# Kernel optimization log

Measured on AMD Instinct MI355X. Metric: run time of the kernel, lower is better.

The kernel has to match this reference:

```python
import jax, jax.numpy as jnp
import numpy as np

B, T, D = 2, 2048, 1024
NH, NKV, HD = 16, 4, 64
BASE, TSL, QGI = 10000.0, 1024, 1.5
EPS = 1.1920929e-07  # torch.finfo(float32).eps used by F.rms_norm default


def _rope_cos_sin(seq_len, rd):
    # Rotary.forward with self.rd == head_dim (Attn sets rd=0 -> full rotation)
    if seq_len > TSL:  # NTK-style base rescale branch
        nb = BASE * (seq_len / TSL) ** (rd / (rd - 2))
    else:
        nb = BASE
    inv = 1.0 / nb ** (jnp.arange(0, rd, 2, dtype=jnp.float32) / rd)
    fr = jnp.arange(seq_len, dtype=jnp.float32)[:, None] * inv[None, :]
    return jnp.cos(fr)[None, :, None, :], jnp.sin(fr)[None, :, None, :]


def _apply_rope(x, cos, sin):
    h = x.shape[-1] // 2
    x1, x2 = x[..., :h], x[..., h:]
    return jnp.concatenate([x1 * cos + x2 * sin, -x1 * sin + x2 * cos], axis=-1)


def _rms_norm(x):
    return x * jax.lax.rsqrt(jnp.mean(x * x, axis=-1, keepdims=True) + EPS)


def setup_inputs() -> dict:
    key = jax.random.key(0)
    ks = jax.random.split(key, 8)
    s = jnp.float32(0.02)
    return {
        "x": jax.random.normal(ks[0], (B, T, D), jnp.float32),
        "qw": jax.random.normal(ks[1], (NH * HD, D), jnp.float32) * s,
        "kw": jax.random.normal(ks[2], (NKV * HD, D), jnp.float32) * s,
        "vw": jax.random.normal(ks[3], (NKV * HD, D), jnp.float32) * s,
        "ow": jax.random.normal(ks[4], (D, D), jnp.float32) * s,
        "ve": jax.random.normal(ks[5], (B, T, NKV * HD), jnp.float32) * s,
        "v0": jax.random.normal(ks[6], (B, T, NKV, HD), jnp.float32) * s,
        "q_gain": jnp.full((NH,), QGI, jnp.float32),
        "vr_lambda": jnp.array([0.5, 0.5], jnp.float32),
        "gate_w": jnp.zeros((NH, D), jnp.float32),      # nn.init.zeros_
        "gate_b": jnp.full((NH,), 4.0, jnp.float32),    # nn.init.constant_(4.0)
    }


def reference(x, qw, kw, vw, ow, ve, v0, q_gain, vr_lambda, gate_w, gate_b):
    # projections
    q = (x @ qw.T).reshape(B, T, NH, HD)
    k = (x @ kw.T).reshape(B, T, NKV, HD)
    v = (x @ vw.T + ve).reshape(B, T, NKV, HD)
    raw_v = v  # returned when vr=True
    v = vr_lambda[0] * v0 + vr_lambda[1] * v  # value residual
    # qk rms-norm + rope (full head dim since self.rd == 0) + per-head q gain
    q = _rms_norm(q)
    k = _rms_norm(k)
    cos, sin = _rope_cos_sin(T, HD)
    q = _apply_rope(q, cos, sin)
    k = _apply_rope(k, cos, sin)
    q = q * q_gain[None, None, :, None]
    # causal GQA attention (nh query heads share nkv kv heads)
    G = NH // NKV
    qg = q.reshape(B, T, NKV, G, HD)
    scale = 1.0 / np.sqrt(HD).astype(np.float32)
    scores = jnp.einsum('bqhgd,bkhd->bhgqk', qg, k) * scale  # [B,NKV,G,T,T]
    causal = jnp.tril(jnp.ones((T, T), bool))
    scores = jnp.where(causal[None, None, None], scores, jnp.finfo(scores.dtype).min)
    p = jax.nn.softmax(scores, axis=-1)
    y = jnp.einsum('bhgqk,bkhd->bqhgd', p, v).reshape(B, T, NH, HD)
    # gated attention output
    gate = jax.nn.sigmoid(x @ gate_w.T + gate_b)  # [B,T,NH]
    y = y * gate[..., None]
    out = y.reshape(B, T, D) @ ow.T
    return out, raw_v
```

## Files before the change

### kernel.cpp

```cpp
#include <hip/hip_runtime.h>
#include <math.h>

#define BB 2
#define TT 2048
#define DD 1024
#define NH 16
#define NKV 4
#define HD 64
#define EPSF 1.1920929e-07f
#define LOG2_NB 14.319970444065578
#define SCALE_LOG2E 0.18033688011112042f
#define FIXMAX 17.5f

typedef __attribute__((ext_vector_type(8))) short bf16x8;
typedef __attribute__((ext_vector_type(4))) float f32x4;

__device__ inline short f2bf(float f) {
    unsigned u = __builtin_bit_cast(unsigned, f);
    unsigned r = (u + 0x7fffu + ((u >> 16) & 1u)) >> 16;
    return (short)r;
}
__device__ inline float bf2f(short s) {
    unsigned u = ((unsigned)(unsigned short)s) << 16;
    return __builtin_bit_cast(float, u);
}
__device__ inline unsigned cvt_pk_bf16(float a, float b) {
    unsigned r;
    asm("v_cvt_pk_bf16_f32 %0, %1, %2" : "=v"(r) : "v"(a), "v"(b));
    return r;
}

__global__ __launch_bounds__(256) void conv_all(
    const float* __restrict__ x, const float* __restrict__ qw,
    const float* __restrict__ kw, const float* __restrict__ vw,
    const float* __restrict__ ow, const float* __restrict__ gw,
    short* __restrict__ x16, short* __restrict__ wb16, short* __restrict__ ow16)
{
    int i = blockIdx.x * 256 + threadIdx.x;
    if (i >= 1708032) {
        ((short4*)(wb16 + 1552*1024))[i - 1708032] = (short4){0,0,0,0};
        return;
    }
    const float* src; short* dst; int j;
    if (i < 1048576)      { src = x;  dst = x16;            j = i; }
    else if (i < 1310720) { src = qw; dst = wb16;           j = i - 1048576; }
    else if (i < 1376256) { src = kw; dst = wb16 + 1048576; j = i - 1310720; }
    else if (i < 1441792) { src = vw; dst = wb16 + 1310720; j = i - 1376256; }
    else if (i < 1703936) { src = ow; dst = ow16;           j = i - 1441792; }
    else                  { src = gw; dst = wb16 + 1572864; j = i - 1703936; }
    float4 v = ((const float4*)src)[j];
    short4 o;
    o.x = f2bf(v.x); o.y = f2bf(v.y); o.z = f2bf(v.z); o.w = f2bf(v.w);
    ((short4*)dst)[j] = o;
}

#define GSTAGE(buf, k0, Abase, Bbase)                                                   \
{                                                                                       \
    _Pragma("unroll")                                                                   \
    for (int i_ = 0; i_ < 2; i_++) {                                                    \
        int off = w*2048 + i_*1024;                      \
        int g = (off >> 4) + lane;                                   \
        int row = g >> 2, c = g & 3;                                                    \
        int cg = c ^ (row & 3);                                        \
        const short* ga = (Abase) + (size_t)(m0 + row)*1024 + (k0) + cg*8;              \
        __builtin_amdgcn_global_load_lds(                                               \
            (const __attribute__((address_space(1))) void*)ga,                          \
            (__attribute__((address_space(3))) void*)((char*)&As[buf][0] + off), 16, 0, 0); \
        const short* gb = (Bbase) + (size_t)(n0 + row)*1024 + (k0) + cg*8;              \
        __builtin_amdgcn_global_load_lds(                                               \
            (const __attribute__((address_space(1))) void*)gb,                          \
            (__attribute__((address_space(3))) void*)((char*)&Bs[buf][0] + off), 16, 0, 0); \
    }                                                                                   \
}

#define GEMM_MAIN_LOOP(kbeg, kend, Abase, Bbase)                                        \
    GSTAGE(0, (kbeg), (Abase), (Bbase));                                                \
    __syncthreads();                                                                    \
    for (int k0 = (kbeg); k0 < (kend); k0 += 32) {                                      \
        int cur = ((k0 - (kbeg)) >> 5) & 1;                                             \
        bf16x8 af[4], bfr[4];                                                           \
        _Pragma("unroll")                                                               \
        for (int tm = 0; tm < 4; tm++) {                                                \
            int row = wy*64 + tm*16 + lc;                                               \
            af[tm] = *(const bf16x8*)(&As[cur][0] + row*32 + ((quad*8) ^ ((row&3)*8))); \
        }                                                                               \
        _Pragma("unroll")                                                               \
        for (int tn = 0; tn < 4; tn++) {                                                \
            int row = wx*64 + tn*16 + lc;                                               \
            bfr[tn] = *(const bf16x8*)(&Bs[cur][0] + row*32 + ((quad*8) ^ ((row&3)*8))); \
        }                                                                               \
        if (k0 + 32 < (kend)) GSTAGE(cur ^ 1, k0 + 32, (Abase), (Bbase));               \
        _Pragma("unroll")                                                               \
        for (int tm = 0; tm < 4; tm++)                                                  \
            _Pragma("unroll")                                                           \
            for (int tn = 0; tn < 4; tn++)                                              \
                acc[tm][tn] = __builtin_amdgcn_mfma_f32_16x16x32_bf16(af[tm], bfr[tn], acc[tm][tn], 0, 0, 0); \
        __syncthreads();                                                                \
    }

__global__ __launch_bounds__(256, 3) void gemm_qkv_fused(
    const short* __restrict__ A, const short* __restrict__ Bmat,
    const float* __restrict__ ve, const float* __restrict__ v0,
    const float* __restrict__ q_gain, const float* __restrict__ vr_lambda,
    const float* __restrict__ gb_, float* __restrict__ gate,
    short* __restrict__ qbh, short* __restrict__ kbh, short* __restrict__ vtb,
    float* __restrict__ rawv)
{
    __shared__ short As[2][128*32];
    __shared__ short Bs[2][128*32];
    int tid = threadIdx.x;
    int w = tid >> 6, lane = tid & 63;
    int quad = lane >> 4, lc = lane & 15;
    int wy = w >> 1, wx = w & 1;
    int m0 = blockIdx.y * 128, n0 = blockIdx.x * 128;

    f32x4 acc[4][4];
    #pragma unroll
    for (int i = 0; i < 4; i++)
        #pragma unroll
        for (int j = 0; j < 4; j++) acc[i][j] = (f32x4){0.f,0.f,0.f,0.f};

    GEMM_MAIN_LOOP(0, 1024, A, Bmat);

    int hc = n0 + wx*64;
    if (hc < 1280) {
        bool isq = (hc < 1024);
        int h = isq ? (hc >> 6) : ((hc - 1024) >> 6);
        float gsc = isq ? (q_gain[h] * SCALE_LOG2E) : 1.0f;
        short* dst = isq ? qbh : kbh;
        int nhh = isq ? 16 : 4;
        float inv0 = (float)exp2((double)lc * (-LOG2_NB / 32.0));
        float inv1 = (float)exp2((double)(lc + 16) * (-LOG2_NB / 32.0));
        #pragma unroll
        for (int tm = 0; tm < 4; tm++) {
            #pragma unroll
            for (int r = 0; r < 4; r++) {
                int m = m0 + wy*64 + tm*16 + quad*4 + r;
                int b = m >> 11, t = m & (TT - 1);
                float a0 = acc[tm][0][r], a1 = acc[tm][1][r];
                float a2 = acc[tm][2][r], a3 = acc[tm][3][r];
                float ss = a0*a0 + a1*a1 + a2*a2 + a3*a3;
                ss += __shfl_xor(ss, 1);
                ss += __shfl_xor(ss, 2);
                ss += __shfl_xor(ss, 4);
                ss += __shfl_xor(ss, 8);
                float rn = rsqrtf(ss * (1.0f/64.0f) + EPSF);
                a0 *= rn; a1 *= rn; a2 *= rn; a3 *= rn;
                float sn0, cs0, sn1, cs1;
                sincosf((float)t * inv0, &sn0, &cs0);
                sincosf((float)t * inv1, &sn1, &cs1);
                float o0 = a0*cs0 + a2*sn0;
                float o1 = a1*cs1 + a3*sn1;
                float o2 = a2*cs0 - a0*sn0;
                float o3 = a3*cs1 - a1*sn1;
                size_t base = (((size_t)(b*nhh + h))*2048 + t)*64 + lc;
                dst[base +  0] = f2bf(o0 * gsc);
                dst[base + 16] = f2bf(o1 * gsc);
                dst[base + 32] = f2bf(o2 * gsc);
                dst[base + 48] = f2bf(o3 * gsc);
            }
        }
    } else if (hc < 1536) {
        int kvh = (hc - 1280) >> 6;
        float l0 = vr_lambda[0], l1 = vr_lambda[1];
        short* lbase = (w < 2) ? &As[w][0] : &Bs[w - 2][0];
        #pragma unroll
        for (int tm = 0; tm < 4; tm++) {
            #pragma unroll
            for (int r = 0; r < 4; r++) {
                int m = m0 + wy*64 + tm*16 + quad*4 + r;
                int tl = tm*16 + quad*4 + r;
                size_t off = (size_t)m*256 + kvh*64 + lc;
                #pragma unroll
                for (int tn = 0; tn < 4; tn++) {
                    int d = tn*16 + lc;
                    float val = acc[tm][tn][r] + ve[off + tn*16];
                    rawv[off + tn*16] = val;
                    lbase[d*64 + (tl ^ ((d & 7) * 8))] = f2bf(l0 * v0[off + tn*16] + l1 * val);
                }
            }
        }
        int b = m0 >> 11;
        int t0g = (m0 & 2047) + wy*64;
        short* vdst = vtb + (size_t)(b*4 + kvh)*64*2048;
        #pragma unroll
        for (int j = 0; j < 16; j++) {
            int d = quad + j*4;
            int tc = lc*4;
            short4 vv = *(const short4*)&lbase[d*64 + (tc ^ ((d & 7) * 8))];
            *(short4*)&vdst[(size_t)d*2048 + t0g + tc] = vv;
        }
    } else if (hc == 1536) {
        #pragma unroll
        for (int tm = 0; tm < 4; tm++)
            #pragma unroll
            for (int r = 0; r < 4; r++) {
                int m = m0 + wy*64 + tm*16 + quad*4 + r;
                float lg = acc[tm][0][r] + gb_[lc];
                gate[(size_t)m*16 + lc] = 1.0f / (1.0f + __expf(-lg));
            }
    }
}

__global__ __launch_bounds__(256, 4) void gemm_mfma(
    const short* __restrict__ A, const short* __restrict__ Bmat,
    float* __restrict__ C, int ldc, int klen)
{
    __shared__ short As[2][128*32];
    __shared__ short Bs[2][128*32];
    int tid = threadIdx.x;
    int w = tid >> 6, lane = tid & 63;
    int quad = lane >> 4, lc = lane & 15;
    int wy = w >> 1, wx = w & 1;
    int m0 = blockIdx.y * 128, n0 = blockIdx.x * 128;

    f32x4 acc[4][4];
    #pragma unroll
    for (int i = 0; i < 4; i++)
        #pragma unroll
        for (int j = 0; j < 4; j++) acc[i][j] = (f32x4){0.f,0.f,0.f,0.f};

    GEMM_MAIN_LOOP(0, klen, A, Bmat);

    #pragma unroll
    for (int tm = 0; tm < 4; tm++)
        #pragma unroll
        for (int r = 0; r < 4; r++) {
            int m = m0 + wy*64 + tm*16 + quad*4 + r;
            #pragma unroll
            for (int tn = 0; tn < 4; tn++) {
                int n = n0 + wx*64 + tn*16 + lc;
                C[(size_t)m*ldc + n] = acc[tm][tn][r];
            }
        }
}

__global__ __launch_bounds__(256, 4) void flash_mfma(
    const short* __restrict__ qbh, const short* __restrict__ kbh,
    const short* __restrict__ vtb, const float* __restrict__ gate,
    short* __restrict__ y16)
{
    __shared__ short Ks[2][64*64];
    __shared__ short Vt[2][64*64];
    __shared__ short Ps[4][16*64];

    int bh = blockIdx.x;
    int b = bh >> 4, h = bh & 15, kvh = h >> 2;
    int qt = 31 - blockIdx.y;
    int tid = threadIdx.x;
    int w = tid >> 6, lane = tid & 63;
    int quad = lane >> 4, lc = lane & 15;

    const short* qbase = qbh + (((size_t)bh)*2048 + qt*64 + w*16 + lc)*64;
    bf16x8 qf0 = *(const bf16x8*)(qbase + quad*8);
    bf16x8 qf1 = *(const bf16x8*)(qbase + 32 + quad*8);

    f32x4 o[4];
    #pragma unroll
    for (int i = 0; i < 4; i++) o[i] = (f32x4){0.f,0.f,0.f,0.f};
    f32x4 l4 = (f32x4){0.f,0.f,0.f,0.f};
    const bf16x8 ones = {(short)0x3F80,(short)0x3F80,(short)0x3F80,(short)0x3F80,
                         (short)0x3F80,(short)0x3F80,(short)0x3F80,(short)0x3F80};

    const size_t kbase = ((size_t)(b*4 + kvh))*2048*64;
    const size_t vbase = ((size_t)(b*4 + kvh))*64*2048;

    #define STAGE(buf, kt)                                                              \
    {                                                                                   \
        _Pragma("unroll")                                                               \
        for (int i = 0; i < 2; i++) {                                                   \
            int off = w*2048 + i*1024;                                                  \
            int g = (off >> 4) + lane;                                                  \
            int row = g >> 3, c = g & 7;                                                \
            int cg = c ^ (row & 7);                                                     \
            const short* gk = kbh + kbase + (size_t)((kt)*64 + row)*64 + cg*8;          \
            __builtin_amdgcn_global_load_lds(                                           \
                (const __attribute__((address_space(1))) void*)gk,                      \
                (__attribute__((address_space(3))) void*)((char*)Ks[buf] + off), 16, 0, 0); \
            const short* gv = vtb + vbase + (size_t)row*2048 + (kt)*64 + cg*8;          \
            __builtin_amdgcn_global_load_lds(                                           \
                (const __attribute__((address_space(1))) void*)gv,                      \
                (__attribute__((address_space(3))) void*)((char*)Vt[buf] + off), 16, 0, 0); \
        }                                                                               \
    }

    STAGE(0, 0);
    __syncthreads();

    short* ps = Ps[w];

    for (int kt = 0; kt <= qt; kt++) {
        int cur = kt & 1;
        bool diag = (kt == qt);

        bf16x8 kf0[4], kf1[4], vf0[4], vf1[4];
        #pragma unroll
        for (int kn = 0; kn < 4; kn++) {
            int row = kn*16 + lc;
            int sw = (row & 7) * 8;
            const short* kr = Ks[cur] + row*64;
            kf0[kn] = *(const bf16x8*)(kr + ((quad*8) ^ sw));
            kf1[kn] = *(const bf16x8*)(kr + ((quad*8 + 32) ^ sw));
            const short* vr = Vt[cur] + row*64;
            vf0[kn] = *(const bf16x8*)(vr + ((quad*8) ^ sw));
            vf1[kn] = *(const bf16x8*)(vr + ((quad*8 + 32) ^ sw));
        }
        if (kt < qt) STAGE(cur ^ 1, kt + 1);

        f32x4 s4[4];
        #pragma unroll
        for (int kn = 0; kn < 4; kn++) {
            f32x4 acc = (f32x4){0.f,0.f,0.f,0.f};
            acc = __builtin_amdgcn_mfma_f32_16x16x32_bf16(kf0[kn], qf0, acc, 0, 0, 0);
            acc = __builtin_amdgcn_mfma_f32_16x16x32_bf16(kf1[kn], qf1, acc, 0, 0, 0);
            s4[kn] = acc;
        }

        #pragma unroll
        for (int kn = 0; kn < 4; kn++) {
            float p0 = __builtin_amdgcn_exp2f(s4[kn][0] - FIXMAX);
            float p1 = __builtin_amdgcn_exp2f(s4[kn][1] - FIXMAX);
            float p2 = __builtin_amdgcn_exp2f(s4[kn][2] - FIXMAX);
            float p3 = __builtin_amdgcn_exp2f(s4[kn][3] - FIXMAX);
            if (diag) {
                int keyb = kn*16 + quad*4, qv = w*16 + lc;
                if (keyb + 0 > qv) p0 = 0.f;
                if (keyb + 1 > qv) p1 = 0.f;
                if (keyb + 2 > qv) p2 = 0.f;
                if (keyb + 3 > qv) p3 = 0.f;
            }
            int c = kn*4 + quad;
            int cs = c ^ ((lc & 7) << 1);
            int2 pk;
            pk.x = (int)cvt_pk_bf16(p0, p1);
            pk.y = (int)cvt_pk_bf16(p2, p3);
            *(int2*)(ps + lc*64 + cs*4) = pk;
        }
        __asm__ volatile("s_waitcnt lgkmcnt(0)" ::: "memory");
        int u0 = (0*4 + quad) ^ (lc & 7);
        int u1 = (1*4 + quad) ^ (lc & 7);
        bf16x8 pf0 = *(const bf16x8*)(ps + lc*64 + u0*8);
        bf16x8 pf1 = *(const bf16x8*)(ps + lc*64 + u1*8);

        #pragma unroll
        for (int dn = 0; dn < 4; dn++) {
            o[dn] = __builtin_amdgcn_mfma_f32_16x16x32_bf16(pf0, vf0[dn], o[dn], 0, 0, 0);
            o[dn] = __builtin_amdgcn_mfma_f32_16x16x32_bf16(pf1, vf1[dn], o[dn], 0, 0, 0);
        }
        l4 = __builtin_amdgcn_mfma_f32_16x16x32_bf16(pf0, ones, l4, 0, 0, 0);
        l4 = __builtin_amdgcn_mfma_f32_16x16x32_bf16(pf1, ones, l4, 0, 0, 0);
        __syncthreads();
    }

    #pragma unroll
    for (int r = 0; r < 4; r++) {
        int row = b*2048 + qt*64 + w*16 + quad*4 + r;
        float g = gate[(size_t)row*16 + h] / l4[r];
        #pragma unroll
        for (int dn = 0; dn < 4; dn++)
            y16[(size_t)row*1024 + h*64 + dn*16 + lc] = f2bf(o[dn][r] * g);
    }
}

extern "C" void kernel_launch(void* const* d_in, const int* in_sizes, int n_in,
                              void* d_out, int out_size, void* d_ws, size_t ws_size,
                              hipStream_t stream) {
    (void)in_sizes; (void)n_in; (void)out_size; (void)ws_size;
    const float* x  = (const float*)d_in[0];
    const float* qw = (const float*)d_in[1];
    const float* kw = (const float*)d_in[2];
    const float* vw = (const float*)d_in[3];
    const float* ow = (const float*)d_in[4];
    const float* ve = (const float*)d_in[5];
    const float* v0 = (const float*)d_in[6];
    const float* qg = (const float*)d_in[7];
    const float* vl = (const float*)d_in[8];
    const float* gw = (const float*)d_in[9];
    const float* gb = (const float*)d_in[10];

    float* out  = (float*)d_out;
    float* rawv = out + (size_t)BB*TT*DD;

    float* p    = (float*)d_ws;
    short* x16  = (short*)p;        p += 2097152;
    short* wb16 = (short*)p;        p += 851968;
    short* ow16 = (short*)p;        p += 524288;
    short* qbh  = (short*)p;        p += 2097152;
    short* kbh  = (short*)p;        p += 524288;
    short* vtb  = (short*)p;        p += 524288;
    float* gt   = p;                p += 65536;
    short* y16  = (short*)p;

    conv_all<<<6784, 256, 0, stream>>>(x, qw, kw, vw, ow, gw, x16, wb16, ow16);
    gemm_qkv_fused<<<dim3(13, 32), 256, 0, stream>>>(x16, wb16, ve, v0, qg, vl,
                                                     gb, gt, qbh, kbh, vtb, rawv);
    flash_mfma<<<dim3(32, 32), 256, 0, stream>>>(qbh, kbh, vtb, gt, y16);
    gemm_mfma<<<dim3(8, 32), 256, 0, stream>>>(y16, ow16, out, 1024, 1024);
}
```

Before: 186.1 us.

## Fuse fp32-to-bf16 conversion into QKV GEMM staging and drop conv kernel

Result: no change. 184.5 us (-0.9%).

```diff
diff --git a/kernel.cpp b/kernel.cpp
--- a/kernel.cpp
+++ b/kernel.cpp
@@ -20,38 +20,10 @@
     unsigned r = (u + 0x7fffu + ((u >> 16) & 1u)) >> 16;
     return (short)r;
 }
-__device__ inline float bf2f(short s) {
-    unsigned u = ((unsigned)(unsigned short)s) << 16;
-    return __builtin_bit_cast(float, u);
-}
 __device__ inline unsigned cvt_pk_bf16(float a, float b) {
     unsigned r;
     asm("v_cvt_pk_bf16_f32 %0, %1, %2" : "=v"(r) : "v"(a), "v"(b));
     return r;
-}
-
-__global__ __launch_bounds__(256) void conv_all(
-    const float* __restrict__ x, const float* __restrict__ qw,
-    const float* __restrict__ kw, const float* __restrict__ vw,
-    const float* __restrict__ ow, const float* __restrict__ gw,
-    short* __restrict__ x16, short* __restrict__ wb16, short* __restrict__ ow16)
-{
-    int i = blockIdx.x * 256 + threadIdx.x;
-    if (i >= 1708032) {
-        ((short4*)(wb16 + 1552*1024))[i - 1708032] = (short4){0,0,0,0};
-        return;
-    }
-    const float* src; short* dst; int j;
-    if (i < 1048576)      { src = x;  dst = x16;            j = i; }
-    else if (i < 1310720) { src = qw; dst = wb16;           j = i - 1048576; }
-    else if (i < 1376256) { src = kw; dst = wb16 + 1048576; j = i - 1310720; }
-    else if (i < 1441792) { src = vw; dst = wb16 + 1310720; j = i - 1376256; }
-    else if (i < 1703936) { src = ow; dst = ow16;           j = i - 1441792; }
-    else                  { src = gw; dst = wb16 + 1572864; j = i - 1703936; }
-    float4 v = ((const float4*)src)[j];
-    short4 o;
-    o.x = f2bf(v.x); o.y = f2bf(v.y); o.z = f2bf(v.z); o.w = f2bf(v.w);
-    ((short4*)dst)[j] = o;
 }
 
 #define GSTAGE(buf, k0, Abase, Bbase)                                                   \
@@ -98,13 +70,15 @@
         __syncthreads();                                                                \
     }
 
-__global__ __launch_bounds__(256, 3) void gemm_qkv_fused(
-    const short* __restrict__ A, const short* __restrict__ Bmat,
+__global__ __launch_bounds__(256, 2) void gemm_qkv_fused(
+    const float* __restrict__ x, const float* __restrict__ qw,
+    const float* __restrict__ kw, const float* __restrict__ vw,
+    const float* __restrict__ gw, const float* __restrict__ ow,
     const float* __restrict__ ve, const float* __restrict__ v0,
     const float* __restrict__ q_gain, const float* __restrict__ vr_lambda,
     const float* __restrict__ gb_, float* __restrict__ gate,
     short* __restrict__ qbh, short* __restrict__ kbh, short* __restrict__ vtb,
-    float* __restrict__ rawv)
+    float* __restrict__ rawv, short* __restrict__ ow16)
 {
     __shared__ short As[2][128*32];
     __shared__ short Bs[2][128*32];
@@ -114,13 +88,100 @@
     int wy = w >> 1, wx = w & 1;
     int m0 = blockIdx.y * 128, n0 = blockIdx.x * 128;
 
+    int g0 = w*128 + lane;
+    int g1 = w*128 + 64 + lane;
+    int rA0 = g0 >> 2, rA1 = g1 >> 2;
+    int cg0 = (g0 & 3) ^ (rA0 & 3);
+    int cg1 = (g1 & 3) ^ (rA1 & 3);
+    const float* aptr0 = x + (size_t)(m0 + rA0)*1024 + cg0*8;
+    const float* aptr1 = x + (size_t)(m0 + rA1)*1024 + cg1*8;
+    int nB0 = n0 + rA0, nB1 = n0 + rA1;
+    const float* bptr0;
+    if      (nB0 < 1024) bptr0 = qw + (size_t)nB0*1024;
+    else if (nB0 < 1280) bptr0 = kw + (size_t)(nB0-1024)*1024;
+    else if (nB0 < 1536) bptr0 = vw + (size_t)(nB0-1280)*1024;
+    else                 bptr0 = gw + (size_t)((nB0-1536)&15)*1024;
+    const float* bptr1;
+    if      (nB1 < 1024) bptr1 = qw + (size_t)nB1*1024;
+    else if (nB1 < 1280) bptr1 = kw + (size_t)(nB1-1024)*1024;
+    else if (nB1 < 1536) bptr1 = vw + (size_t)(nB1-1280)*1024;
+    else                 bptr1 = gw + (size_t)((nB1-1536)&15)*1024;
+    bptr0 += cg0*8; bptr1 += cg1*8;
+    unsigned bmask0 = (nB0 < 1552) ? 0xFFFFFFFFu : 0u;
+    unsigned bmask1 = (nB1 < 1552) ? 0xFFFFFFFFu : 0u;
+
+    float4 A0a, A0b, A1a, A1b, B0a, B0b, B1a, B1b;
+
+    #define QSTG_LOAD(k0)                                                   \
+    {                                                                       \
+        A0a = *(const float4*)(aptr0 + (k0));                               \
+        A0b = *(const float4*)(aptr0 + (k0) + 4);                           \
+        A1a = *(const float4*)(aptr1 + (k0));                               \
+        A1b = *(const float4*)(aptr1 + (k0) + 4);                           \
+        B0a = *(const float4*)(bptr0 + (k0));                               \
+        B0b = *(const float4*)(bptr0 + (k0) + 4);                           \
+        B1a = *(const float4*)(bptr1 + (k0));                               \
+        B1b = *(const float4*)(bptr1 + (k0) + 4);                           \
+    }
+
+    #define QSTG_WRITE(buf)                                                 \
+    {                                                                       \
+        unsigned q0, q1, q2, q3; int4 pk;                                   \
+        q0 = cvt_pk_bf16(A0a.x, A0a.y); q1 = cvt_pk_bf16(A0a.z, A0a.w);     \
+        q2 = cvt_pk_bf16(A0b.x, A0b.y); q3 = cvt_pk_bf16(A0b.z, A0b.w);     \
+        pk = (int4){(int)q0,(int)q1,(int)q2,(int)q3};                       \
+        *(int4*)((char*)&As[buf][0] + w*2048 + lane*16) = pk;               \
+        q0 = cvt_pk_bf16(A1a.x, A1a.y); q1 = cvt_pk_bf16(A1a.z, A1a.w);     \
+        q2 = cvt_pk_bf16(A1b.x, A1b.y); q3 = cvt_pk_bf16(A1b.z, A1b.w);     \
+        pk = (int4){(int)q0,(int)q1,(int)q2,(int)q3};                       \
+        *(int4*)((char*)&As[buf][0] + w*2048 + 1024 + lane*16) = pk;        \
+        q0 = cvt_pk_bf16(B0a.x, B0a.y) & bmask0;                            \
+        q1 = cvt_pk_bf16(B0a.z, B0a.w) & bmask0;                            \
+        q2 = cvt_pk_bf16(B0b.x, B0b.y) & bmask0;                            \
+        q3 = cvt_pk_bf16(B0b.z, B0b.w) & bmask0;                            \
+        pk = (int4){(int)q0,(int)q1,(int)q2,(int)q3};                       \
+        *(int4*)((char*)&Bs[buf][0] + w*2048 + lane*16) = pk;               \
+        q0 = cvt_pk_bf16(B1a.x, B1a.y) & bmask1;                            \
+        q1 = cvt_pk_bf16(B1a.z, B1a.w) & bmask1;                            \
+        q2 = cvt_pk_bf16(B1b.x, B1b.y) & bmask1;                            \
+        q3 = cvt_pk_bf16(B1b.z, B1b.w) & bmask1;                            \
+        pk = (int4){(int)q0,(int)q1,(int)q2,(int)q3};                       \
+        *(int4*)((char*)&Bs[buf][0] + w*2048 + 1024 + lane*16) = pk;        \
+    }
+
     f32x4 acc[4][4];
     #pragma unroll
     for (int i = 0; i < 4; i++)
         #pragma unroll
         for (int j = 0; j < 4; j++) acc[i][j] = (f32x4){0.f,0.f,0.f,0.f};
 
-    GEMM_MAIN_LOOP(0, 1024, A, Bmat);
+    QSTG_LOAD(0);
+    QSTG_WRITE(0);
+    __syncthreads();
+
+    for (int k0 = 0; k0 < 1024; k0 += 32) {
+        int cur = (k0 >> 5) & 1;
+        bool pre = (k0 + 32) < 1024;
+        bf16x8 af[4], bfr[4];
+        #pragma unroll
+        for (int tm = 0; tm < 4; tm++) {
+            int row = wy*64 + tm*16 + lc;
+            af[tm] = *(const bf16x8*)(&As[cur][0] + row*32 + ((quad*8) ^ ((row&3)*8)));
+        }
+        #pragma unroll
+        for (int tn = 0; tn < 4; tn++) {
+            int row = wx*64 + tn*16 + lc;
+            bfr[tn] = *(const bf16x8*)(&Bs[cur][0] + row*32 + ((quad*8) ^ ((row&3)*8)));
+        }
+        if (pre) QSTG_LOAD(k0 + 32);
+        #pragma unroll
+        for (int tm = 0; tm < 4; tm++)
+            #pragma unroll
+            for (int tn = 0; tn < 4; tn++)
+                acc[tm][tn] = __builtin_amdgcn_mfma_f32_16x16x32_bf16(af[tm], bfr[tn], acc[tm][tn], 0, 0, 0);
+        if (pre) QSTG_WRITE(cur ^ 1);
+        __syncthreads();
+    }
 
     int hc = n0 + wx*64;
     if (hc < 1280) {
@@ -200,6 +261,16 @@
                 gate[(size_t)m*16 + lc] = 1.0f / (1.0f + __expf(-lg));
             }
     }
+
+    int gtid = (blockIdx.y * 13 + blockIdx.x) * 256 + tid;
+    for (int idx = gtid; idx < 262144; idx += 106496) {
+        float4 v = ((const float4*)ow)[idx];
+        short4 o;
+        o.x = f2bf(v.x); o.y = f2bf(v.y); o.z = f2bf(v.z); o.w = f2bf(v.w);
+        ((short4*)ow16)[idx] = o;
+    }
+    #undef QSTG_LOAD
+    #undef QSTG_WRITE
 }
 
 __global__ __launch_bounds__(256, 4) void gemm_mfma(
@@ -382,8 +453,6 @@
     float* rawv = out + (size_t)BB*TT*DD;
 
     float* p    = (float*)d_ws;
-    short* x16  = (short*)p;        p += 2097152;
-    short* wb16 = (short*)p;        p += 851968;
     short* ow16 = (short*)p;        p += 524288;
     short* qbh  = (short*)p;        p += 2097152;
     short* kbh  = (short*)p;        p += 524288;
@@ -391,9 +460,9 @@
     float* gt   = p;                p += 65536;
     short* y16  = (short*)p;
 
-    conv_all<<<6784, 256, 0, stream>>>(x, qw, kw, vw, ow, gw, x16, wb16, ow16);
-    gemm_qkv_fused<<<dim3(13, 32), 256, 0, stream>>>(x16, wb16, ve, v0, qg, vl,
-                                                     gb, gt, qbh, kbh, vtb, rawv);
+    gemm_qkv_fused<<<dim3(13, 32), 256, 0, stream>>>(x, qw, kw, vw, gw, ow,
+                                                     ve, v0, qg, vl, gb, gt,
+                                                     qbh, kbh, vtb, rawv, ow16);
     flash_mfma<<<dim3(32, 32), 256, 0, stream>>>(qbh, kbh, vtb, gt, y16);
     gemm_mfma<<<dim3(8, 32), 256, 0, stream>>>(y16, ow16, out, 1024, 1024);
 }
```

## Fuse fp32-to-bf16 conversion into QKV GEMM loads and drop conv kernel

Applied to the files above, without the earlier changes.

After: 197.7 us. 6.2% more time.

```diff
diff --git a/kernel.cpp b/kernel.cpp
--- a/kernel.cpp
+++ b/kernel.cpp
@@ -20,38 +20,18 @@
     unsigned r = (u + 0x7fffu + ((u >> 16) & 1u)) >> 16;
     return (short)r;
 }
-__device__ inline float bf2f(short s) {
-    unsigned u = ((unsigned)(unsigned short)s) << 16;
-    return __builtin_bit_cast(float, u);
-}
 __device__ inline unsigned cvt_pk_bf16(float a, float b) {
     unsigned r;
     asm("v_cvt_pk_bf16_f32 %0, %1, %2" : "=v"(r) : "v"(a), "v"(b));
     return r;
 }
-
-__global__ __launch_bounds__(256) void conv_all(
-    const float* __restrict__ x, const float* __restrict__ qw,
-    const float* __restrict__ kw, const float* __restrict__ vw,
-    const float* __restrict__ ow, const float* __restrict__ gw,
-    short* __restrict__ x16, short* __restrict__ wb16, short* __restrict__ ow16)
-{
-    int i = blockIdx.x * 256 + threadIdx.x;
-    if (i >= 1708032) {
-        ((short4*)(wb16 + 1552*1024))[i - 1708032] = (short4){0,0,0,0};
-        return;
-    }
-    const float* src; short* dst; int j;
-    if (i < 1048576)      { src = x;  dst = x16;            j = i; }
-    else if (i < 1310720) { src = qw; dst = wb16;           j = i - 1048576; }
-    else if (i < 1376256) { src = kw; dst = wb16 + 1048576; j = i - 1310720; }
-    else if (i < 1441792) { src = vw; dst = wb16 + 1310720; j = i - 1376256; }
-    else if (i < 1703936) { src = ow; dst = ow16;           j = i - 1441792; }
-    else                  { src = gw; dst = wb16 + 1572864; j = i - 1703936; }
-    float4 v = ((const float4*)src)[j];
-    short4 o;
-    o.x = f2bf(v.x); o.y = f2bf(v.y); o.z = f2bf(v.z); o.w = f2bf(v.w);
-    ((short4*)dst)[j] = o;
+__device__ inline bf16x8 cvt_frag(float4 a, float4 b, unsigned msk) {
+    int4 pk;
+    pk.x = (int)(cvt_pk_bf16(a.x, a.y) & msk);
+    pk.y = (int)(cvt_pk_bf16(a.z, a.w) & msk);
+    pk.z = (int)(cvt_pk_bf16(b.x, b.y) & msk);
+    pk.w = (int)(cvt_pk_bf16(b.z, b.w) & msk);
+    return __builtin_bit_cast(bf16x8, pk);
 }
 
 #define GSTAGE(buf, k0, Abase, Bbase)                                                   \
@@ -98,21 +78,57 @@
         __syncthreads();                                                                \
     }
 
-__global__ __launch_bounds__(256, 3) void gemm_qkv_fused(
-    const short* __restrict__ A, const short* __restrict__ Bmat,
+__global__ __launch_bounds__(256, 2) void gemm_qkv_fused(
+    const float* __restrict__ x, const float* __restrict__ qw,
+    const float* __restrict__ kw, const float* __restrict__ vw,
+    const float* __restrict__ gw, const float* __restrict__ ow,
     const float* __restrict__ ve, const float* __restrict__ v0,
     const float* __restrict__ q_gain, const float* __restrict__ vr_lambda,
     const float* __restrict__ gb_, float* __restrict__ gate,
     short* __restrict__ qbh, short* __restrict__ kbh, short* __restrict__ vtb,
-    float* __restrict__ rawv)
+    float* __restrict__ rawv, short* __restrict__ ow16)
 {
-    __shared__ short As[2][128*32];
-    __shared__ short Bs[2][128*32];
+    __shared__ float Asf[2][128*32];
+    __shared__ float Bsf[2][128*32];
     int tid = threadIdx.x;
     int w = tid >> 6, lane = tid & 63;
     int quad = lane >> 4, lc = lane & 15;
     int wy = w >> 1, wx = w & 1;
-    int m0 = blockIdx.y * 128, n0 = blockIdx.x * 128;
+    int m0 = blockIdx.x * 128, n0 = blockIdx.y * 128;
+
+    const float* asrc[4]; const float* bsrc[4]; int ldst[4];
+    #pragma unroll
+    for (int i = 0; i < 4; i++) {
+        int g = w*256 + i*64 + lane;
+        int row = g >> 3, c = g & 7;
+        int cg = c ^ (row & 7);
+        asrc[i] = x + (size_t)(m0 + row)*1024 + cg*4;
+        int nB = n0 + row;
+        const float* bp;
+        if      (nB < 1024) bp = qw + (size_t)nB*1024;
+        else if (nB < 1280) bp = kw + (size_t)(nB-1024)*1024;
+        else if (nB < 1536) bp = vw + (size_t)(nB-1280)*1024;
+        else                bp = gw + (size_t)((nB-1536)&15)*1024;
+        bsrc[i] = bp + cg*4;
+        ldst[i] = w*4096 + i*1024;
+    }
+    unsigned bmsk[4];
+    #pragma unroll
+    for (int tn = 0; tn < 4; tn++)
+        bmsk[tn] = (n0 + wx*64 + tn*16 < 1552) ? 0xFFFFFFFFu : 0u;
+
+    #define STAGEF(buf, k0)                                                             \
+    {                                                                                   \
+        _Pragma("unroll")                                                               \
+        for (int i_ = 0; i_ < 4; i_++) {                                                \
+            __builtin_amdgcn_global_load_lds(                                           \
+                (const __attribute__((address_space(1))) void*)(asrc[i_] + (k0)),       \
+                (__attribute__((address_space(3))) void*)((char*)&Asf[buf][0] + ldst[i_]), 16, 0, 0); \
+            __builtin_amdgcn_global_load_lds(                                           \
+                (const __attribute__((address_space(1))) void*)(bsrc[i_] + (k0)),       \
+                (__attribute__((address_space(3))) void*)((char*)&Bsf[buf][0] + ldst[i_]), 16, 0, 0); \
+        }                                                                               \
+    }
 
     f32x4 acc[4][4];
     #pragma unroll
@@ -120,7 +136,38 @@
         #pragma unroll
         for (int j = 0; j < 4; j++) acc[i][j] = (f32x4){0.f,0.f,0.f,0.f};
 
-    GEMM_MAIN_LOOP(0, 1024, A, Bmat);
+    STAGEF(0, 0);
+    __syncthreads();
+
+    for (int k0 = 0; k0 < 1024; k0 += 32) {
+        int cur = (k0 >> 5) & 1;
+        bf16x8 af[4], bfr[4];
+        #pragma unroll
+        for (int tm = 0; tm < 4; tm++) {
+            int row = wy*64 + tm*16 + lc;
+            int r7 = row & 7;
+            const float* rp = &Asf[cur][row*32];
+            float4 fa = *(const float4*)(rp + (((2*quad)   ^ r7) * 4));
+            float4 fb = *(const float4*)(rp + (((2*quad+1) ^ r7) * 4));
+            af[tm] = cvt_frag(fa, fb, 0xFFFFFFFFu);
+        }
+        #pragma unroll
+        for (int tn = 0; tn < 4; tn++) {
+            int row = wx*64 + tn*16 + lc;
+            int r7 = row & 7;
+            const float* rp = &Bsf[cur][row*32];
+            float4 fa = *(const float4*)(rp + (((2*quad)   ^ r7) * 4));
+            float4 fb = *(const float4*)(rp + (((2*quad+1) ^ r7) * 4));
+            bfr[tn] = cvt_frag(fa, fb, bmsk[tn]);
+        }
+        if (k0 + 32 < 1024) STAGEF(cur ^ 1, k0 + 32);
+        #pragma unroll
+        for (int tm = 0; tm < 4; tm++)
+            #pragma unroll
+            for (int tn = 0; tn < 4; tn++)
+                acc[tm][tn] = __builtin_amdgcn_mfma_f32_16x16x32_bf16(af[tm], bfr[tn], acc[tm][tn], 0, 0, 0);
+        __syncthreads();
+    }
 
     int hc = n0 + wx*64;
     if (hc < 1280) {
@@ -163,7 +210,7 @@
     } else if (hc < 1536) {
         int kvh = (hc - 1280) >> 6;
         float l0 = vr_lambda[0], l1 = vr_lambda[1];
-        short* lbase = (w < 2) ? &As[w][0] : &Bs[w - 2][0];
+        short* lbase = (short*)((char*)&Asf[0][0] + w*8192);
         #pragma unroll
         for (int tm = 0; tm < 4; tm++) {
             #pragma unroll
@@ -200,6 +247,15 @@
                 gate[(size_t)m*16 + lc] = 1.0f / (1.0f + __expf(-lg));
             }
     }
+
+    int gtid = (blockIdx.y * 32 + blockIdx.x) * 256 + tid;
+    for (int idx = gtid; idx < 262144; idx += 106496) {
+        float4 v = ((const float4*)ow)[idx];
+        short4 o;
+        o.x = f2bf(v.x); o.y = f2bf(v.y); o.z = f2bf(v.z); o.w = f2bf(v.w);
+        ((short4*)ow16)[idx] = o;
+    }
+    #undef STAGEF
 }
 
 __global__ __launch_bounds__(256, 4) void gemm_mfma(
@@ -382,8 +438,6 @@
     float* rawv = out + (size_t)BB*TT*DD;
 
     float* p    = (float*)d_ws;
-    short* x16  = (short*)p;        p += 2097152;
-    short* wb16 = (short*)p;        p += 851968;
     short* ow16 = (short*)p;        p += 524288;
     short* qbh  = (short*)p;        p += 2097152;
     short* kbh  = (short*)p;        p += 524288;
@@ -391,9 +445,9 @@
     float* gt   = p;                p += 65536;
     short* y16  = (short*)p;
 
-    conv_all<<<6784, 256, 0, stream>>>(x, qw, kw, vw, ow, gw, x16, wb16, ow16);
-    gemm_qkv_fused<<<dim3(13, 32), 256, 0, stream>>>(x16, wb16, ve, v0, qg, vl,
-                                                     gb, gt, qbh, kbh, vtb, rawv);
+    gemm_qkv_fused<<<dim3(32, 13), 256, 0, stream>>>(x, qw, kw, vw, gw, ow,
+                                                     ve, v0, qg, vl, gb, gt,
+                                                     qbh, kbh, vtb, rawv, ow16);
     flash_mfma<<<dim3(32, 32), 256, 0, stream>>>(qbh, kbh, vtb, gt, y16);
     gemm_mfma<<<dim3(8, 32), 256, 0, stream>>>(y16, ow16, out, 1024, 1024);
 }
```

## Triple-buffer QKV GEMM loads with vmcnt waits and swap grid block order

Applied to the files above, without the earlier changes.

New measurement: 176.8 us. 5.0% less time.

```diff
diff --git a/kernel.cpp b/kernel.cpp
--- a/kernel.cpp
+++ b/kernel.cpp
@@ -19,10 +19,6 @@
     unsigned u = __builtin_bit_cast(unsigned, f);
     unsigned r = (u + 0x7fffu + ((u >> 16) & 1u)) >> 16;
     return (short)r;
-}
-__device__ inline float bf2f(short s) {
-    unsigned u = ((unsigned)(unsigned short)s) << 16;
-    return __builtin_bit_cast(float, u);
 }
 __device__ inline unsigned cvt_pk_bf16(float a, float b) {
     unsigned r;
@@ -54,7 +50,7 @@
     ((short4*)dst)[j] = o;
 }
 
-#define GSTAGE(buf, k0, Abase, Bbase)                                                   \
+#define GSTAGE(Abuf, Bbuf, k0, Abase, Bbase)                                            \
 {                                                                                       \
     _Pragma("unroll")                                                                   \
     for (int i_ = 0; i_ < 2; i_++) {                                                    \
@@ -65,16 +61,16 @@
         const short* ga = (Abase) + (size_t)(m0 + row)*1024 + (k0) + cg*8;              \
         __builtin_amdgcn_global_load_lds(                                               \
             (const __attribute__((address_space(1))) void*)ga,                          \
-            (__attribute__((address_space(3))) void*)((char*)&As[buf][0] + off), 16, 0, 0); \
+            (__attribute__((address_space(3))) void*)((char*)(Abuf) + off), 16, 0, 0);  \
         const short* gb = (Bbase) + (size_t)(n0 + row)*1024 + (k0) + cg*8;              \
         __builtin_amdgcn_global_load_lds(                                               \
             (const __attribute__((address_space(1))) void*)gb,                          \
-            (__attribute__((address_space(3))) void*)((char*)&Bs[buf][0] + off), 16, 0, 0); \
+            (__attribute__((address_space(3))) void*)((char*)(Bbuf) + off), 16, 0, 0);  \
     }                                                                                   \
 }
 
 #define GEMM_MAIN_LOOP(kbeg, kend, Abase, Bbase)                                        \
-    GSTAGE(0, (kbeg), (Abase), (Bbase));                                                \
+    GSTAGE(&As[0][0], &Bs[0][0], (kbeg), (Abase), (Bbase));                             \
     __syncthreads();                                                                    \
     for (int k0 = (kbeg); k0 < (kend); k0 += 32) {                                      \
         int cur = ((k0 - (kbeg)) >> 5) & 1;                                             \
@@ -89,7 +85,7 @@
             int row = wx*64 + tn*16 + lc;                                               \
             bfr[tn] = *(const bf16x8*)(&Bs[cur][0] + row*32 + ((quad*8) ^ ((row&3)*8))); \
         }                                                                               \
-        if (k0 + 32 < (kend)) GSTAGE(cur ^ 1, k0 + 32, (Abase), (Bbase));               \
+        if (k0 + 32 < (kend)) GSTAGE(&As[cur^1][0], &Bs[cur^1][0], k0 + 32, (Abase), (Bbase)); \
         _Pragma("unroll")                                                               \
         for (int tm = 0; tm < 4; tm++)                                                  \
             _Pragma("unroll")                                                           \
@@ -106,13 +102,13 @@
     short* __restrict__ qbh, short* __restrict__ kbh, short* __restrict__ vtb,
     float* __restrict__ rawv)
 {
-    __shared__ short As[2][128*32];
-    __shared__ short Bs[2][128*32];
+    __shared__ short As[3][128*32];
+    __shared__ short Bs[3][128*32];
     int tid = threadIdx.x;
     int w = tid >> 6, lane = tid & 63;
     int quad = lane >> 4, lc = lane & 15;
     int wy = w >> 1, wx = w & 1;
-    int m0 = blockIdx.y * 128, n0 = blockIdx.x * 128;
+    int m0 = blockIdx.x * 128, n0 = blockIdx.y * 128;
 
     f32x4 acc[4][4];
     #pragma unroll
@@ -120,7 +116,36 @@
         #pragma unroll
         for (int j = 0; j < 4; j++) acc[i][j] = (f32x4){0.f,0.f,0.f,0.f};
 
-    GEMM_MAIN_LOOP(0, 1024, A, Bmat);
+    GSTAGE(&As[0][0], &Bs[0][0], 0,  A, Bmat);
+    GSTAGE(&As[1][0], &Bs[1][0], 32, A, Bmat);
+
+    for (int k0 = 0; k0 < 1024; k0 += 32) {
+        int st = k0 >> 5;
+        int cur = st % 3;
+        if (st < 31) asm volatile("s_waitcnt vmcnt(4)\n\ts_barrier" ::: "memory");
+        else         asm volatile("s_waitcnt vmcnt(0)\n\ts_barrier" ::: "memory");
+        bf16x8 af[4], bfr[4];
+        #pragma unroll
+        for (int tm = 0; tm < 4; tm++) {
+            int row = wy*64 + tm*16 + lc;
+            af[tm] = *(const bf16x8*)(&As[cur][0] + row*32 + ((quad*8) ^ ((row&3)*8)));
+        }
+        #pragma unroll
+        for (int tn = 0; tn < 4; tn++) {
+            int row = wx*64 + tn*16 + lc;
+            bfr[tn] = *(const bf16x8*)(&Bs[cur][0] + row*32 + ((quad*8) ^ ((row&3)*8)));
+        }
+        if (k0 + 64 < 1024) {
+            int nxt = (st + 2) % 3;
+            GSTAGE(&As[nxt][0], &Bs[nxt][0], k0 + 64, A, Bmat);
+        }
+        #pragma unroll
+        for (int tm = 0; tm < 4; tm++)
+            #pragma unroll
+            for (int tn = 0; tn < 4; tn++)
+                acc[tm][tn] = __builtin_amdgcn_mfma_f32_16x16x32_bf16(af[tm], bfr[tn], acc[tm][tn], 0, 0, 0);
+    }
+    __syncthreads();
 
     int hc = n0 + wx*64;
     if (hc < 1280) {
@@ -163,7 +188,8 @@
     } else if (hc < 1536) {
         int kvh = (hc - 1280) >> 6;
         float l0 = vr_lambda[0], l1 = vr_lambda[1];
-        short* lbase = (w < 2) ? &As[w][0] : &Bs[w - 2][0];
+        short* lbase = (w < 3) ? (short*)((char*)&As[0][0] + w*8192)
+                               : (short*)&Bs[0][0];
         #pragma unroll
         for (int tm = 0; tm < 4; tm++) {
             #pragma unroll
@@ -392,7 +418,7 @@
     short* y16  = (short*)p;
 
     conv_all<<<6784, 256, 0, stream>>>(x, qw, kw, vw, ow, gw, x16, wb16, ow16);
-    gemm_qkv_fused<<<dim3(13, 32), 256, 0, stream>>>(x16, wb16, ve, v0, qg, vl,
+    gemm_qkv_fused<<<dim3(32, 13), 256, 0, stream>>>(x16, wb16, ve, v0, qg, vl,
                                                      gb, gt, qbh, kbh, vtb, rawv);
     flash_mfma<<<dim3(32, 32), 256, 0, stream>>>(qbh, kbh, vtb, gt, y16);
     gemm_mfma<<<dim3(8, 32), 256, 0, stream>>>(y16, ow16, out, 1024, 1024);
```
